# Kernel tuning notes

Measured on AMD Instinct MI355X. Metric: run time of the kernel, lower is better.

Reference implementation:

```python
import jax, jax.numpy as jnp
import numpy as np

TEMPERATURE = 8.0  # sqrt(head_dim=64)


def setup_inputs() -> dict:
    key = jax.random.key(0)
    kq, kk, kv, km = jax.random.split(key, 4)
    B, S, D = 16, 2048, 64
    q = jax.random.normal(kq, (B, S, D), dtype=jnp.float32)
    k = jax.random.normal(kk, (B, S, D), dtype=jnp.float32)
    v = jax.random.normal(kv, (B, S, D), dtype=jnp.float32)
    mask = jax.random.randint(km, (B, S, S), 0, 2).astype(jnp.bool_)
    return {"q": q, "k": k, "v": v, "mask": mask}


def reference(q, k, v, mask):
    # latent = q @ k^T / temperature  -> [B, Sq, Sk]
    latent = jnp.einsum('bqd,bkd->bqk', q, k) / TEMPERATURE
    # NOTE: the original fills masked positions with 1e-9 (NOT -inf); keep faithful.
    latent = jnp.where(mask, jnp.float32(1e-9), latent)
    attn = jax.nn.softmax(latent, axis=-1)
    return jnp.einsum('bqk,bkd->bqd', attn, v)
```

## Files before the change

### kernel.cpp

```cpp
#include <hip/hip_runtime.h>
#include <hip/hip_bf16.h>

#define BB 16
#define SS 2048
#define DD 64
#define NT_TILES (SS / 128)
#define TILE_BYTES 16384

typedef __attribute__((ext_vector_type(8)))  unsigned short ushort8;
typedef __attribute__((ext_vector_type(8)))  __bf16 bf16x8;
typedef __attribute__((ext_vector_type(16))) float f32x16;
typedef __attribute__((ext_vector_type(4)))  unsigned int uint4v;

static __device__ __forceinline__ unsigned short f2bf(float x) {
    return __builtin_bit_cast(unsigned short, __float2bfloat16(x));
}
static __device__ __forceinline__ unsigned pk2(float a, float b) {
    return (unsigned)f2bf(a) | ((unsigned)f2bf(b) << 16);
}
union F4 { float4 v; float a[4]; };

#define GLDS16(src, dst) __builtin_amdgcn_global_load_lds(                 \
    (const __attribute__((address_space(1))) unsigned int*)(src),          \
    (__attribute__((address_space(3))) unsigned int*)(dst), 16, 0, 0)

__global__ __launch_bounds__(256)
void prepack_kernel(const float* __restrict__ K, const float* __restrict__ V,
                    char* __restrict__ wsK, char* __restrict__ wsV) {
    __shared__ __align__(16) char smem[32768];
    char* Ks = smem;
    char* Vs = smem + 16384;
    const int t  = threadIdx.x;
    const int kt = blockIdx.x;
    const int b  = blockIdx.y;
    const float* Kg = K + (size_t)b * SS * DD;
    const float* Vg = V + (size_t)b * SS * DD;

    #pragma unroll
    for (int j = 0; j < 4; j++) {
        const int idx = 2 * t + 512 * j;
        const int row = idx >> 4;
        const int g   = (idx & 15) >> 1;
        const float* src = Kg + (size_t)(kt * 128) * DD + (size_t)idx * 4;
        F4 fa, fb; fa.v = *(const float4*)src; fb.v = *(const float4*)(src + 4);
        ushort8 u;
        #pragma unroll
        for (int e = 0; e < 4; e++) { u[e] = f2bf(fa.a[e]); u[e + 4] = f2bf(fb.a[e]); }
        *(ushort8*)(Ks + row * 128 + ((g ^ (row & 7)) * 16)) = u;
    }
    {
        const int d0v = (t & 15) * 4;
        const int kkb = (t >> 4) * 4;
        #pragma unroll
        for (int it2 = 0; it2 < 2; it2++) {
            const int kk = kkb + 64 * it2;
            const float* src = Vg + (size_t)(kt * 128 + kk) * DD + d0v;
            F4 r0, r1, r2, r3;
            r0.v = *(const float4*)(src);
            r1.v = *(const float4*)(src + DD);
            r2.v = *(const float4*)(src + 2 * DD);
            r3.v = *(const float4*)(src + 3 * DD);
            #pragma unroll
            for (int e = 0; e < 4; e++) {
                const int d = d0v + e;
                const uint2 wv = make_uint2(pk2(r0.a[e], r1.a[e]), pk2(r2.a[e], r3.a[e]));
                *(uint2*)(Vs + d * 256 + (((kk >> 3) ^ (d & 15)) * 16) + (kk & 7) * 2) = wv;
            }
        }
    }
    __syncthreads();
    char* dK = wsK + (size_t)(b * NT_TILES + kt) * TILE_BYTES;
    char* dV = wsV + (size_t)(b * NT_TILES + kt) * TILE_BYTES;
    #pragma unroll
    for (int j = 0; j < 4; j++) {
        *(float4*)(dK + t * 16 + j * 4096) = *(const float4*)(Ks + t * 16 + j * 4096);
        *(float4*)(dV + t * 16 + j * 4096) = *(const float4*)(Vs + t * 16 + j * 4096);
    }
}

struct KTile { bf16x8 ak[4]; };

__global__ __launch_bounds__(256, 3)
void sdpa_mfma_kernel(const float* __restrict__ Q, const char* __restrict__ wsK,
                      const char* __restrict__ wsV, const unsigned int* __restrict__ M,
                      float* __restrict__ O) {
    __shared__ __align__(16) char smem[49152];
    char* Qs = smem;
    float* red  = (float*)smem;
    float* denx = (float*)(smem + 24576);

    const int t    = threadIdx.x;
    const int lane = t & 63;
    const int l31  = lane & 31;
    const int half = lane >> 5;
    const int kh   = t >> 6;
    const int b    = blockIdx.y;
    const int q0   = blockIdx.x * 32;

    {
        const int sr = t >> 3, sc = t & 7;
        const float* src = Q + ((size_t)b * SS + q0 + sr) * DD + sc * 8;
        F4 f0, f1; f0.v = *(const float4*)src; f1.v = *(const float4*)(src + 4);
        ushort8 u;
        #pragma unroll
        for (int e = 0; e < 4; e++) {
            u[e]     = f2bf(f0.a[e] * 0.125f);
            u[e + 4] = f2bf(f1.a[e] * 0.125f);
        }
        *(ushort8*)(Qs + sr * 128 + ((sc ^ (sr & 7)) * 16)) = u;
    }
    __syncthreads();

    const int qrow = l31;
    bf16x8 bq[4];
    #pragma unroll
    for (int dc = 0; dc < 4; dc++)
        bq[dc] = __builtin_bit_cast(bf16x8, *(const ushort8*)(
            Qs + qrow * 128 + (((2 * dc + half) ^ (qrow & 7)) * 16)));
    __syncthreads();

    f32x16 On0, On1;
    #pragma unroll
    for (int i = 0; i < 16; i++) { On0[i] = 0.f; On1[i] = 0.f; }
    float den0 = 0.f, den1 = 0.f;

    const int krow = 32 * kh + l31;
    const char* tKbase = wsK + (size_t)b * NT_TILES * TILE_BYTES;
    const char* tVbase = wsV + (size_t)b * NT_TILES * TILE_BYTES;

    const unsigned int* Msrc = M + (size_t)b * SS * SS
                                 + (size_t)(q0 + (lane >> 3)) * SS
                                 + 32 * kh + 4 * ((lane & 7) ^ (lane >> 3));
    char* const wbase = smem + kh * 4096;

    auto stage = [&](int bufn, int kt) {
        const unsigned int* src = Msrc + (size_t)kt * 128;
        char* dst = wbase + bufn * 16384;
        #pragma unroll
        for (int j = 0; j < 4; j++)
            GLDS16(src + (size_t)j * 8 * SS, dst + j * 1024);
    };

    auto load_kt = [&](KTile& T, int kt) {
        const char* tK = tKbase + (size_t)kt * TILE_BYTES;
        #pragma unroll
        for (int dc = 0; dc < 4; dc++)
            T.ak[dc] = __builtin_bit_cast(bf16x8, *(const ushort8*)(
                tK + krow * 128 + (((2 * dc + half) ^ (krow & 7)) * 16)));
    };

    const int r7 = l31 & 7;

    auto tile_body = [&](const KTile& cur, KTile& nxt, int kt, int ktS, int ktnK) {
        stage((kt + 2) % 3, ktS);
        asm volatile("s_waitcnt vmcnt(8)" ::: "memory");
        __builtin_amdgcn_sched_barrier(0);

        uint4v mt[4];
        const char* mb = smem + (kt % 3) * 16384 + kh * 4096 + l31 * 128;
        #pragma unroll
        for (int g = 0; g < 4; g++)
            mt[g] = *(const uint4v*)(mb + 16 * ((half + 2 * g) ^ r7));

        const char* tV = tVbase + (size_t)kt * TILE_BYTES;
        bf16x8 av[2][2];
        #pragma unroll
        for (int s2 = 0; s2 < 2; s2++)
            #pragma unroll
            for (int dc = 0; dc < 2; dc++) {
                const int vrow = 32 * dc + l31;
                av[s2][dc] = __builtin_bit_cast(bf16x8, *(const ushort8*)(
                    tV + vrow * 256 + (((4 * kh + 2 * s2 + half) ^ (vrow & 15)) * 16)));
            }
        load_kt(nxt, ktnK);

        f32x16 S;
        #pragma unroll
        for (int i = 0; i < 16; i++) S[i] = 0.f;
        #pragma unroll
        for (int dc = 0; dc < 4; dc++)
            S = __builtin_amdgcn_mfma_f32_32x32x16_bf16(cur.ak[dc], bq[dc], S, 0, 0, 0);

        float p[16];
        #pragma unroll
        for (int g = 0; g < 4; g++) {
            #pragma unroll
            for (int e = 0; e < 4; e++) {
                const float ev = __expf(S[4 * g + e]);
                const float pv = mt[g][e] ? 1.0f : ev;
                p[4 * g + e] = pv;
                if (g & 1) den1 += pv; else den0 += pv;
            }
        }

        #pragma unroll
        for (int s2 = 0; s2 < 2; s2++) {
            const unsigned o0 = pk2(p[8 * s2 + 0], p[8 * s2 + 1]);
            const unsigned o1 = pk2(p[8 * s2 + 2], p[8 * s2 + 3]);
            const unsigned o2 = pk2(p[8 * s2 + 4], p[8 * s2 + 5]);
            const unsigned o3 = pk2(p[8 * s2 + 6], p[8 * s2 + 7]);
            const unsigned s0 = half ? o0 : o2;
            const unsigned s1 = half ? o1 : o3;
            const unsigned r0 = (unsigned)__shfl_xor((int)s0, 32, 64);
            const unsigned r1 = (unsigned)__shfl_xor((int)s1, 32, 64);
            uint4 bu;
            bu.x = half ? r0 : o0;
            bu.y = half ? r1 : o1;
            bu.z = half ? o2 : r0;
            bu.w = half ? o3 : r1;
            const bf16x8 bp = __builtin_bit_cast(bf16x8, bu);
            On0 = __builtin_amdgcn_mfma_f32_32x32x16_bf16(av[s2][0], bp, On0, 0, 0, 0);
            On1 = __builtin_amdgcn_mfma_f32_32x32x16_bf16(av[s2][1], bp, On1, 0, 0, 0);
        }
    };

    KTile KA, KB;
    load_kt(KA, 0);
    stage(0, 0);
    stage(1, 1);
    #pragma unroll 1
    for (int kt = 0; kt < NT_TILES; kt += 2) {
        const int kA = (kt + 2 < NT_TILES) ? (kt + 2) : (NT_TILES - 1);
        const int kB = (kt + 3 < NT_TILES) ? (kt + 3) : (NT_TILES - 1);
        tile_body(KA, KB, kt,     kA, kt + 1);
        tile_body(KB, KA, kt + 1, kB, kA);
    }

    const float den_acc = den0 + den1;
    const float den_tot = den_acc + __shfl_xor(den_acc, 32, 64);

    __syncthreads();
    if (kh != 0) {
        #pragma unroll
        for (int dc = 0; dc < 2; dc++)
            #pragma unroll
            for (int g = 0; g < 4; g++) {
                const f32x16& Oc = dc ? On1 : On0;
                float4 st;
                st.x = Oc[4 * g + 0]; st.y = Oc[4 * g + 1];
                st.z = Oc[4 * g + 2]; st.w = Oc[4 * g + 3];
                *(float4*)((char*)red + (kh - 1) * 8192 + (dc * 4 + g) * 1024 + lane * 16) = st;
            }
        if (lane < 32) denx[kh * 32 + l31] = den_tot;
    }
    __syncthreads();
    if (kh == 0) {
        const float inv = 1.0f / (den_tot + denx[32 + l31] + denx[64 + l31] + denx[96 + l31]);
        float* Og = O + ((size_t)b * SS + q0 + qrow) * DD;
        #pragma unroll
        for (int dc = 0; dc < 2; dc++)
            #pragma unroll
            for (int g = 0; g < 4; g++) {
                const f32x16& Oc = dc ? On1 : On0;
                float4 st;
                st.x = Oc[4 * g + 0]; st.y = Oc[4 * g + 1];
                st.z = Oc[4 * g + 2]; st.w = Oc[4 * g + 3];
                #pragma unroll
                for (int w2 = 0; w2 < 3; w2++) {
                    const float4 pr = *(const float4*)((char*)red + w2 * 8192 +
                                                       (dc * 4 + g) * 1024 + lane * 16);
                    st.x += pr.x; st.y += pr.y; st.z += pr.z; st.w += pr.w;
                }
                st.x *= inv; st.y *= inv; st.z *= inv; st.w *= inv;
                *(float4*)(Og + 32 * dc + 8 * g + 4 * half) = st;
            }
    }
}

extern "C" void kernel_launch(void* const* d_in, const int* in_sizes, int n_in,
                              void* d_out, int out_size, void* d_ws, size_t ws_size,
                              hipStream_t stream) {
    const float* q = (const float*)d_in[0];
    const float* k = (const float*)d_in[1];
    const float* v = (const float*)d_in[2];
    const unsigned int* m = (const unsigned int*)d_in[3];
    float* out = (float*)d_out;

    char* wsK = (char*)d_ws;
    char* wsV = wsK + (size_t)BB * NT_TILES * TILE_BYTES;

    dim3 pgrid(NT_TILES, BB);
    prepack_kernel<<<pgrid, 256, 0, stream>>>(k, v, wsK, wsV);

    dim3 grid(SS / 32, BB);
    sdpa_mfma_kernel<<<grid, 256, 0, stream>>>(q, wsK, wsV, m, out);
}
```

Baseline: 415.8 us.

## Stage K and V tiles through LDS via async global_load_lds alongside mask

K and V tiles are no longer read straight from global into registers (K double-buffered in registers, V loaded per tile). They now go through LDS with global_load_lds in the same three-stage async pipeline as the mask, and the loop is simplified to a single tile per iteration. The goal is to hide K/V global latency behind the mask pipeline and drop the register-resident K prefetch. In exchange, LDS use grows from 48 KB to 144 KB per block and launch_bounds drops to one block per CU, which sharply reduces occupancy.

```diff
diff --git a/kernel.cpp b/kernel.cpp
--- a/kernel.cpp
+++ b/kernel.cpp
@@ -6,6 +6,7 @@
 #define DD 64
 #define NT_TILES (SS / 128)
 #define TILE_BYTES 16384
+#define BUF_BYTES 49152
 
 typedef __attribute__((ext_vector_type(8)))  unsigned short ushort8;
 typedef __attribute__((ext_vector_type(8)))  __bf16 bf16x8;
@@ -78,13 +79,11 @@
     }
 }
 
-struct KTile { bf16x8 ak[4]; };
-
-__global__ __launch_bounds__(256, 3)
+__global__ __launch_bounds__(256, 1)
 void sdpa_mfma_kernel(const float* __restrict__ Q, const char* __restrict__ wsK,
                       const char* __restrict__ wsV, const unsigned int* __restrict__ M,
                       float* __restrict__ O) {
-    __shared__ __align__(16) char smem[49152];
+    __shared__ __align__(16) char smem[3 * BUF_BYTES];
     char* Qs = smem;
     float* red  = (float*)smem;
     float* denx = (float*)(smem + 24576);
@@ -124,45 +123,54 @@
     for (int i = 0; i < 16; i++) { On0[i] = 0.f; On1[i] = 0.f; }
     float den0 = 0.f, den1 = 0.f;
 
-    const int krow = 32 * kh + l31;
     const char* tKbase = wsK + (size_t)b * NT_TILES * TILE_BYTES;
     const char* tVbase = wsV + (size_t)b * NT_TILES * TILE_BYTES;
 
     const unsigned int* Msrc = M + (size_t)b * SS * SS
                                  + (size_t)(q0 + (lane >> 3)) * SS
                                  + 32 * kh + 4 * ((lane & 7) ^ (lane >> 3));
-    char* const wbase = smem + kh * 4096;
+    const int voff = ((lane >> 2) * 256)
+                   + ((kh ^ ((lane >> 4) & 3)) * 64)
+                   + (((lane & 3) ^ ((lane >> 2) & 3)) * 16);
+    const int r7 = l31 & 7;
 
     auto stage = [&](int bufn, int kt) {
-        const unsigned int* src = Msrc + (size_t)kt * 128;
-        char* dst = wbase + bufn * 16384;
+        char* wb = smem + bufn * BUF_BYTES + kh * 12288;
+        const char* tK = tKbase + (size_t)kt * TILE_BYTES + 32 * kh * 128;
         #pragma unroll
         for (int j = 0; j < 4; j++)
-            GLDS16(src + (size_t)j * 8 * SS, dst + j * 1024);
+            GLDS16(tK + j * 1024 + lane * 16, wb + j * 1024);
+        const char* tV = tVbase + (size_t)kt * TILE_BYTES;
+        #pragma unroll
+        for (int j = 0; j < 4; j++)
+            GLDS16(tV + j * 4096 + voff, wb + 4096 + j * 1024);
+        const unsigned int* ms = Msrc + (size_t)kt * 128;
+        #pragma unroll
+        for (int j = 0; j < 4; j++)
+            GLDS16(ms + (size_t)j * 8 * SS, wb + 8192 + j * 1024);
     };
 
-    auto load_kt = [&](KTile& T, int kt) {
-        const char* tK = tKbase + (size_t)kt * TILE_BYTES;
+    stage(0, 0);
+    stage(1, 1);
+
+    #pragma unroll 1
+    for (int kt = 0; kt < NT_TILES; ++kt) {
+        const int ktS = (kt + 2 < NT_TILES) ? kt + 2 : NT_TILES - 1;
+        stage((kt + 2) % 3, ktS);
+        asm volatile("s_waitcnt vmcnt(24)" ::: "memory");
+        __builtin_amdgcn_sched_barrier(0);
+
+        const char* wb = smem + (kt % 3) * BUF_BYTES + kh * 12288;
+
+        bf16x8 ak[4];
         #pragma unroll
         for (int dc = 0; dc < 4; dc++)
-            T.ak[dc] = __builtin_bit_cast(bf16x8, *(const ushort8*)(
-                tK + krow * 128 + (((2 * dc + half) ^ (krow & 7)) * 16)));
-    };
-
-    const int r7 = l31 & 7;
-
-    auto tile_body = [&](const KTile& cur, KTile& nxt, int kt, int ktS, int ktnK) {
-        stage((kt + 2) % 3, ktS);
-        asm volatile("s_waitcnt vmcnt(8)" ::: "memory");
-        __builtin_amdgcn_sched_barrier(0);
-
+            ak[dc] = __builtin_bit_cast(bf16x8, *(const ushort8*)(
+                wb + l31 * 128 + (((2 * dc + half) ^ r7) * 16)));
         uint4v mt[4];
-        const char* mb = smem + (kt % 3) * 16384 + kh * 4096 + l31 * 128;
         #pragma unroll
         for (int g = 0; g < 4; g++)
-            mt[g] = *(const uint4v*)(mb + 16 * ((half + 2 * g) ^ r7));
-
-        const char* tV = tVbase + (size_t)kt * TILE_BYTES;
+            mt[g] = *(const uint4v*)(wb + 8192 + l31 * 128 + 16 * ((half + 2 * g) ^ r7));
         bf16x8 av[2][2];
         #pragma unroll
         for (int s2 = 0; s2 < 2; s2++)
@@ -170,16 +178,15 @@
             for (int dc = 0; dc < 2; dc++) {
                 const int vrow = 32 * dc + l31;
                 av[s2][dc] = __builtin_bit_cast(bf16x8, *(const ushort8*)(
-                    tV + vrow * 256 + (((4 * kh + 2 * s2 + half) ^ (vrow & 15)) * 16)));
-            }
-        load_kt(nxt, ktnK);
+                    wb + 4096 + vrow * 64 + (2 * s2 + half) * 16));
+            }
 
         f32x16 S;
         #pragma unroll
         for (int i = 0; i < 16; i++) S[i] = 0.f;
         #pragma unroll
         for (int dc = 0; dc < 4; dc++)
-            S = __builtin_amdgcn_mfma_f32_32x32x16_bf16(cur.ak[dc], bq[dc], S, 0, 0, 0);
+            S = __builtin_amdgcn_mfma_f32_32x32x16_bf16(ak[dc], bq[dc], S, 0, 0, 0);
 
         float p[16];
         #pragma unroll
@@ -212,18 +219,6 @@
             On0 = __builtin_amdgcn_mfma_f32_32x32x16_bf16(av[s2][0], bp, On0, 0, 0, 0);
             On1 = __builtin_amdgcn_mfma_f32_32x32x16_bf16(av[s2][1], bp, On1, 0, 0, 0);
         }
-    };
-
-    KTile KA, KB;
-    load_kt(KA, 0);
-    stage(0, 0);
-    stage(1, 1);
-    #pragma unroll 1
-    for (int kt = 0; kt < NT_TILES; kt += 2) {
-        const int kA = (kt + 2 < NT_TILES) ? (kt + 2) : (NT_TILES - 1);
-        const int kB = (kt + 3 < NT_TILES) ? (kt + 3) : (NT_TILES - 1);
-        tile_body(KA, KB, kt,     kA, kt + 1);
-        tile_body(KB, KA, kt + 1, kB, kA);
     }
 
     const float den_acc = den0 + den1;
```

Measured after the change: 393.8 us. -5.3%, faster.
